# Kernel optimization log

Measured on AMD Instinct MI355X. Metric: run time of the kernel, lower is better.

## Reference

```python
import jax, jax.numpy as jnp
import numpy as np

VOCAB, EMBED, ZCH = 4096, 128, 256
B, H, W = 32, 16, 16


def setup_inputs() -> dict:
    key = jax.random.key(0)
    k1, k2, k3, k4 = jax.random.split(key, 4)
    z_e = jax.random.normal(k1, (B, ZCH, H, W), dtype=jnp.float32)
    pre_w = jax.random.normal(k2, (EMBED, ZCH), dtype=jnp.float32) * 0.02
    pre_b = jnp.zeros((EMBED,), dtype=jnp.float32)
    # codebook initialized uniform(-1/vocab, 1/vocab) like the torch module
    emb = jax.random.uniform(k3, (VOCAB, EMBED), dtype=jnp.float32,
                             minval=-1.0 / VOCAB, maxval=1.0 / VOCAB)
    post_w = jax.random.normal(k4, (ZCH, EMBED), dtype=jnp.float32) * 0.02
    post_b = jnp.zeros((ZCH,), dtype=jnp.float32)
    return {"z_e": z_e, "pre_w": pre_w, "pre_b": pre_b, "emb": emb,
            "post_w": post_w, "post_b": post_b}


def reference(z_e, pre_w, pre_b, emb, post_w, post_b):
    # pre_quant_conv: 1x1 conv == per-pixel linear, z_channels -> embed_dim
    z = jnp.einsum('bchw,ec->behw', z_e, pre_w) + pre_b[None, :, None, None]
    b, e, h, w = z.shape
    zf = z.transpose(0, 2, 3, 1).reshape(-1, e)                 # (b*h*w, e)
    # squared distance to all codebook vectors: |z|^2 + |c|^2 - 2 z.c
    dist = (jnp.sum(zf * zf, axis=1, keepdims=True)
            + jnp.sum(emb * emb, axis=1)
            - 2.0 * zf @ emb.T)                                  # (b*h*w, vocab)
    tokens = jnp.argmin(dist, axis=-1)                           # (b*h*w,)
    z_q = emb[tokens].reshape(b, h, w, e).transpose(0, 3, 1, 2)  # (b,e,h,w)
    # straight-through estimator
    dec_in = z + jax.lax.stop_gradient(z_q - z)
    # post_quant_conv: 1x1 conv embed_dim -> z_channels (decoder input)
    rec = jnp.einsum('behw,ce->bchw', dec_in, post_w) + post_b[None, :, None, None]
    return z, z_q, rec
```

## Files before the change

### kernel.cpp

```cpp
#include <hip/hip_runtime.h>
#include <hip/hip_bf16.h>
#include <cstdint>

#define NB   32
#define NC   256
#define NE   128
#define NS   256
#define NV   4096
#define NP   8192
#define NSPLIT 8

typedef unsigned short ushort_t;
typedef __attribute__((ext_vector_type(8))) short bf16x8;
typedef __attribute__((ext_vector_type(8))) unsigned short us8;
typedef __attribute__((ext_vector_type(4))) float f32x4;

__device__ __forceinline__ float bf2f(ushort_t u) {
    union { unsigned int i; float f; } x; x.i = ((unsigned int)u) << 16; return x.f;
}
__device__ __forceinline__ ushort_t f2bf(float f) {
    __hip_bfloat16 h = __float2bfloat16(f);
    ushort_t u; __builtin_memcpy(&u, &h, 2); return u;
}
__device__ __forceinline__ unsigned asu(float f) { unsigned u; __builtin_memcpy(&u,&f,4); return u; }
__device__ __forceinline__ float    asf(unsigned u) { float f; __builtin_memcpy(&f,&u,4); return f; }

__global__ __launch_bounds__(256) void pre_conv_pack(
    const float* __restrict__ z_e, const float* __restrict__ pre_w,
    const float* __restrict__ pre_b, const float* __restrict__ emb,
    float* __restrict__ out_z, ushort_t* __restrict__ Bpack,
    float* __restrict__ cnorm)
{
    __shared__ __align__(16) float wtile[16 * 256];
    __shared__ __align__(16) float part[4 * 16 * 64];

    const int t = threadIdx.x;

    if (blockIdx.x == 8) {
        const int v     = (blockIdx.y * 4 + blockIdx.z) * 32 + (t >> 3);
        const int chunk = t & 7;
        const float4* rp = (const float4*)(emb + (size_t)v * NE + chunk * 16);
        float4 x0 = rp[0], x1 = rp[1], x2 = rp[2], x3 = rp[3];
        float xs[16] = { x0.x, x0.y, x0.z, x0.w, x1.x, x1.y, x1.z, x1.w,
                         x2.x, x2.y, x2.z, x2.w, x3.x, x3.y, x3.z, x3.w };
        us8 h0, h1;
        float nn = 0.f;
#pragma unroll
        for (int j = 0; j < 8; j++) {
            nn = fmaf(xs[j], xs[j], nn);
            h0[j] = f2bf(xs[j]);
        }
#pragma unroll
        for (int j = 0; j < 8; j++) {
            nn = fmaf(xs[8 + j], xs[8 + j], nn);
            h1[j] = f2bf(xs[8 + j]);
        }
        nn += __shfl_xor(nn, 1);
        nn += __shfl_xor(nn, 2);
        nn += __shfl_xor(nn, 4);
        if (chunk == 0) cnorm[v] = 0.5f * nn;

        const int G  = v >> 4;
        const int ks = chunk >> 1;
        const int q0 = (chunk & 1) * 2;
        const int L0 = (v & 15) | (q0 << 4);
        const int L1 = (v & 15) | ((q0 + 1) << 4);
        *(us8*)(Bpack + ((size_t)G * 4 + ks) * 512 + L0 * 8) = h0;
        *(us8*)(Bpack + ((size_t)G * 4 + ks) * 512 + L1 * 8) = h1;
        return;
    }

    const int e0 = blockIdx.x * 16;
    const int b  = blockIdx.y;
    const int s0 = blockIdx.z * 64;

    for (int idx = t; idx < 16 * 256; idx += 256)
        wtile[idx] = pre_w[(e0 + (idx >> 8)) * 256 + (idx & 255)];
    __syncthreads();

    const int kq = t >> 6, sl = t & 63;
    float acc[16];
#pragma unroll
    for (int r = 0; r < 16; r++) acc[r] = 0.f;

    const float* zin = z_e + (size_t)(b * NC + kq * 64) * NS + s0 + sl;
    const int cb = kq * 64;
#pragma unroll 4
    for (int i = 0; i < 16; i++) {
        const int c = i * 4;
        float z0 = zin[(c + 0) * NS];
        float z1 = zin[(c + 1) * NS];
        float z2 = zin[(c + 2) * NS];
        float z3 = zin[(c + 3) * NS];
#pragma unroll
        for (int r = 0; r < 16; r++) {
            float4 w = *(const float4*)&wtile[r * 256 + cb + c];
            acc[r] = fmaf(z0, w.x, fmaf(z1, w.y, fmaf(z2, w.z, fmaf(z3, w.w, acc[r]))));
        }
    }
#pragma unroll
    for (int r = 0; r < 16; r++)
        part[(kq * 16 + r) * 64 + sl] = acc[r];
    __syncthreads();

    const int r4 = t >> 6, sl2 = t & 63;
#pragma unroll
    for (int j = 0; j < 4; j++) {
        const int r = j * 4 + r4;
        float v = pre_b[e0 + r]
                + part[(0 * 16 + r) * 64 + sl2]
                + part[(1 * 16 + r) * 64 + sl2]
                + part[(2 * 16 + r) * 64 + sl2]
                + part[(3 * 16 + r) * 64 + sl2];
        out_z[(size_t)(b * NE + e0 + r) * NS + s0 + sl2] = v;
    }
}

__global__ __launch_bounds__(256, 3) void score_mfma(
    const float* __restrict__ z, const ushort_t* __restrict__ Bpack,
    const float* __restrict__ cnorm, int* __restrict__ pidx4)
{
    __shared__ __align__(16) char smraw[40960];
    float* As  = (float*)smraw;
    float* r1  = (float*)smraw;
    float* r2  = (float*)(smraw + 16640);
    float* t4b = (float*)(smraw + 33280);

    const int t = threadIdx.x;
    const int wave = t >> 6, lane = t & 63;
    const int set = blockIdx.x;
    const int split = blockIdx.y;
    const int p0 = set * 64;
    const int b  = p0 >> 8;
    const int s0 = p0 & 255;

    for (int idx = t; idx < 64 * 128; idx += 256) {
        int k = idx >> 6, i = idx & 63;
        As[i * 132 + k] = z[(size_t)(b * NE + k) * NS + s0 + i];
    }
    __syncthreads();

    const int am = lane & 15, aq = lane >> 4;
    bf16x8 ah[4][4];
#pragma unroll
    for (int mt = 0; mt < 4; mt++)
#pragma unroll
        for (int ks = 0; ks < 4; ks++) {
            const unsigned* src = (const unsigned*)(As + (mt * 16 + am) * 132 + ks * 32 + aq * 8);
            union { unsigned u[4]; bf16x8 v; } pk;
#pragma unroll
            for (int pr = 0; pr < 4; pr++)
                pk.u[pr] = (src[2 * pr + 1] & 0xFFFF0000u) | (src[2 * pr] >> 16);
            ah[mt][ks] = pk.v;
        }
    __syncthreads();

    const int Gbase = split * 32 + wave * 8;
    float cn[8];
#pragma unroll
    for (int cgi = 0; cgi < 8; cgi++)
        cn[cgi] = cnorm[(Gbase + cgi) * 16 + am];

    float b1v[16], b2v[16];
#pragma unroll
    for (int i = 0; i < 16; i++) { b1v[i] = -1e30f; b2v[i] = -1e30f; }

    bf16x8 bh[4], bhn[4];
#pragma unroll
    for (int ks = 0; ks < 4; ks++)
        bh[ks] = *(const bf16x8*)(Bpack + ((size_t)Gbase * 4 + ks) * 512 + lane * 8);

    for (int cgi = 0; cgi < 8; cgi++) {
        if (cgi < 7) {
#pragma unroll
            for (int ks = 0; ks < 4; ks++)
                bhn[ks] = *(const bf16x8*)(Bpack + ((size_t)(Gbase + cgi + 1) * 4 + ks) * 512 + lane * 8);
        }

        f32x4 acc[4];
#pragma unroll
        for (int mt = 0; mt < 4; mt++) acc[mt] = (f32x4){0.f, 0.f, 0.f, 0.f};
#pragma unroll
        for (int ks = 0; ks < 4; ks++)
#pragma unroll
            for (int mt = 0; mt < 4; mt++)
                acc[mt] = __builtin_amdgcn_mfma_f32_16x16x32_bf16(ah[mt][ks], bh[ks], acc[mt], 0, 0, 0);

#pragma unroll
        for (int mt = 0; mt < 4; mt++)
#pragma unroll
            for (int reg = 0; reg < 4; reg++) {
                const int si = mt * 4 + reg;
                float sc = acc[mt][reg] - cn[cgi];
                float ev = asf((asu(sc) & ~7u) | (unsigned)cgi);
                b2v[si] = fmaxf(b2v[si], fminf(ev, b1v[si]));
                b1v[si] = fmaxf(b1v[si], ev);
            }
#pragma unroll
        for (int ks = 0; ks < 4; ks++) bh[ks] = bhn[ks];
    }

    const int slot = wave * 16 + am;
#pragma unroll
    for (int mt = 0; mt < 4; mt++)
#pragma unroll
        for (int reg = 0; reg < 4; reg++) {
            int px = mt * 16 + aq * 4 + reg;
            r1[slot * 65 + px] = b1v[mt * 4 + reg];
            r2[slot * 65 + px] = b2v[mt * 4 + reg];
        }
    __syncthreads();

    {
        const int px = t >> 2, ch = t & 3;
        float t1 = -1e30f, t2 = -1e30f, t3 = -1e30f, t4 = -1e30f;
        for (int i = 0; i < 16; i++) {
            int sl = ch * 16 + i;
#pragma unroll
            for (int e = 0; e < 2; e++) {
                float raw = e ? r2[sl * 65 + px] : r1[sl * 65 + px];
                unsigned vb = asu(raw);
                float v = asf((vb & ~511u) | ((unsigned)sl << 3) | (vb & 7u));
                t4 = fmaxf(t4, fminf(v, t3));
                t3 = fmaxf(t3, fminf(v, t2));
                t2 = fmaxf(t2, fminf(v, t1));
                t1 = fmaxf(t1, v);
            }
        }
        float* dst = t4b + (px * 4 + ch) * 4;
        dst[0] = t1; dst[1] = t2; dst[2] = t3; dst[3] = t4;
    }
    __syncthreads();

    if (t < 64) {
        float u1 = -1e30f, u2 = -1e30f, u3 = -1e30f, u4 = -1e30f;
        for (int ch = 0; ch < 4; ch++) {
#pragma unroll
            for (int j = 0; j < 4; j++) {
                float v = t4b[(t * 4 + ch) * 4 + j];
                u4 = fmaxf(u4, fminf(v, u3));
                u3 = fmaxf(u3, fminf(v, u2));
                u2 = fmaxf(u2, fminf(v, u1));
                u1 = fmaxf(u1, v);
            }
        }
        const int p = p0 + t;
        float uu[4] = { u1, u2, u3, u4 };
#pragma unroll
        for (int j = 0; j < 4; j++) {
            unsigned bits = asu(uu[j]) & 511u;
            int w = (int)(bits >> 7), res = (int)((bits >> 3) & 15u), cg = (int)(bits & 7u);
            pidx4[((size_t)split * NP + p) * 4 + j] = split * 512 + (w * 8 + cg) * 16 + res;
        }
    }
}

__global__ __launch_bounds__(256) void rescore_gather(
    const float* __restrict__ z, const float* __restrict__ emb,
    const int* __restrict__ pidx4, float* __restrict__ out_zq)
{
    __shared__ __align__(16) float zl[16 * 132];
    __shared__ double bsl[16 * 16];
    __shared__ int    bil[16 * 16];
    __shared__ int    tok[16];

    const int t  = threadIdx.x;
    const int p0 = blockIdx.x * 16;
    const int b  = p0 >> 8;
    const int s0 = p0 & 255;

    for (int idx = t; idx < 16 * 128; idx += 256) {
        int k = idx >> 4, i = idx & 15;
        zl[i * 132 + k] = z[(size_t)(b * NE + k) * NS + s0 + i];
    }
    __syncthreads();

    const int il = t >> 4;
    const int cc = t & 15;
    const int p  = p0 + il;
    double bs = -1e300; int bi = 0x7fffffff;
#pragma unroll
    for (int jj = 0; jj < 2; jj++) {
        int cand = cc * 2 + jj;
        int split = cand >> 2, slot = cand & 3;
        int idx = pidx4[((size_t)split * NP + p) * 4 + slot];
        const float* er = emb + (size_t)idx * NE;
        double dot = 0.0, nn = 0.0;
        for (int k = 0; k < NE; k += 4) {
            float4 e4 = *(const float4*)(er + k);
            dot += (double)zl[il * 132 + k + 0] * (double)e4.x;
            dot += (double)zl[il * 132 + k + 1] * (double)e4.y;
            dot += (double)zl[il * 132 + k + 2] * (double)e4.z;
            dot += (double)zl[il * 132 + k + 3] * (double)e4.w;
            nn  += (double)e4.x * e4.x + (double)e4.y * e4.y
                 + (double)e4.z * e4.z + (double)e4.w * e4.w;
        }
        double sc = dot - 0.5 * nn;
        if (sc > bs || (sc == bs && idx < bi)) { bs = sc; bi = idx; }
    }
    bsl[il * 16 + cc] = bs;
    bil[il * 16 + cc] = bi;
    __syncthreads();

    if (t < 16) {
        double B = -1e300; int I = 0x7fffffff;
        for (int c = 0; c < 16; c++) {
            double sc = bsl[t * 16 + c]; int ii = bil[t * 16 + c];
            if (sc > B || (sc == B && ii < I)) { B = sc; I = ii; }
        }
        tok[t] = I;
    }
    __syncthreads();

    for (int idx = t; idx < NE * 16; idx += 256) {
        int e = idx >> 4, i = idx & 15;
        out_zq[(size_t)(b * NE + e) * NS + s0 + i] = emb[(size_t)tok[i] * NE + e];
    }
}

__global__ __launch_bounds__(256) void post_conv(
    const float* __restrict__ zq, const float* __restrict__ post_w,
    const float* __restrict__ post_b, float* __restrict__ out_rec)
{
    __shared__ __align__(16) float wtile[16 * 128];
    __shared__ __align__(16) float part[4 * 16 * 64];

    const int t  = threadIdx.x;
    const int c0 = blockIdx.x * 16;
    const int b  = blockIdx.y;
    const int s0 = blockIdx.z * 64;

    for (int idx = t; idx < 16 * 128; idx += 256)
        wtile[idx] = post_w[(c0 + (idx >> 7)) * 128 + (idx & 127)];
    __syncthreads();

    const int kq = t >> 6, sl = t & 63;
    float acc[16];
#pragma unroll
    for (int r = 0; r < 16; r++) acc[r] = 0.f;

    const float* zin = zq + (size_t)(b * NE + kq * 32) * NS + s0 + sl;
    const int eb = kq * 32;
#pragma unroll 4
    for (int i = 0; i < 8; i++) {
        const int e = i * 4;
        float z0 = zin[(e + 0) * NS];
        float z1 = zin[(e + 1) * NS];
        float z2 = zin[(e + 2) * NS];
        float z3 = zin[(e + 3) * NS];
#pragma unroll
        for (int r = 0; r < 16; r++) {
            float4 w = *(const float4*)&wtile[r * 128 + eb + e];
            acc[r] = fmaf(z0, w.x, fmaf(z1, w.y, fmaf(z2, w.z, fmaf(z3, w.w, acc[r]))));
        }
    }
#pragma unroll
    for (int r = 0; r < 16; r++)
        part[(kq * 16 + r) * 64 + sl] = acc[r];
    __syncthreads();

    const int r4 = t >> 6, sl2 = t & 63;
#pragma unroll
    for (int j = 0; j < 4; j++) {
        const int r = j * 4 + r4;
        float v = post_b[c0 + r]
                + part[(0 * 16 + r) * 64 + sl2]
                + part[(1 * 16 + r) * 64 + sl2]
                + part[(2 * 16 + r) * 64 + sl2]
                + part[(3 * 16 + r) * 64 + sl2];
        out_rec[(size_t)(b * NC + c0 + r) * NS + s0 + sl2] = v;
    }
}

extern "C" void kernel_launch(void* const* d_in, const int* in_sizes, int n_in,
                              void* d_out, int out_size, void* d_ws, size_t ws_size,
                              hipStream_t stream)
{
    const float* z_e    = (const float*)d_in[0];
    const float* pre_w  = (const float*)d_in[1];
    const float* pre_b  = (const float*)d_in[2];
    const float* emb    = (const float*)d_in[3];
    const float* post_w = (const float*)d_in[4];
    const float* post_b = (const float*)d_in[5];

    float* out     = (float*)d_out;
    float* out_z   = out;
    float* out_zq  = out + 1048576;
    float* out_rec = out + 2097152;

    const size_t SZ_BPACK = (size_t)256 * 4 * 512 * 2;
    const size_t SZ_CNORM = (size_t)NV * 4;
    const size_t SZ_PIDX4 = (size_t)NSPLIT * NP * 4 * 4;
    const size_t NEED = SZ_BPACK + SZ_CNORM + SZ_PIDX4;
    char* scr = (ws_size >= NEED) ? (char*)d_ws : (char*)out_rec;
    ushort_t* Bpack = (ushort_t*)scr;
    float*    cnorm = (float*)(scr + SZ_BPACK);
    int*      pidx4 = (int*)(scr + SZ_BPACK + SZ_CNORM);

    pre_conv_pack <<<dim3(9, 32, 4),     256, 0, stream>>>(z_e, pre_w, pre_b, emb,
                                                           out_z, Bpack, cnorm);
    score_mfma    <<<dim3(128, NSPLIT),  256, 0, stream>>>(out_z, Bpack, cnorm, pidx4);
    rescore_gather<<<dim3(512),          256, 0, stream>>>(out_z, emb, pidx4, out_zq);
    post_conv     <<<dim3(16, 32, 4),    256, 0, stream>>>(out_zq, post_w, post_b, out_rec);
}
```

Before: 151.5 us.

## Fuse four VQ stages into one cooperative persistent kernel with grid syncs

Replaces the four separate launches (pre-conv/pack, MFMA scoring, rescore/gather, post-conv) with one cooperative kernel. The stages are separated by grid.sync and run as grid-stride loops over the same work units. The aim is to remove per-launch overhead and the inter-kernel gaps. The cost is grid-wide barriers, a persistent grid capped at 1024 blocks that may lower parallelism in some stages, and shared-memory sizing fixed to the largest stage. The old multi-kernel path stays as a fallback if the cooperative launch fails.

```diff
diff --git a/kernel.cpp b/kernel.cpp
--- a/kernel.cpp
+++ b/kernel.cpp
@@ -1,6 +1,9 @@
 #include <hip/hip_runtime.h>
 #include <hip/hip_bf16.h>
+#include <hip/hip_cooperative_groups.h>
 #include <cstdint>
+
+namespace cg = cooperative_groups;
 
 #define NB   32
 #define NC   256
@@ -25,6 +28,353 @@
 __device__ __forceinline__ unsigned asu(float f) { unsigned u; __builtin_memcpy(&u,&f,4); return u; }
 __device__ __forceinline__ float    asf(unsigned u) { float f; __builtin_memcpy(&f,&u,4); return f; }
 
+__global__ __launch_bounds__(256, 3) void vq_fused(
+    const float* __restrict__ z_e, const float* __restrict__ pre_w,
+    const float* __restrict__ pre_b, const float* __restrict__ emb,
+    const float* __restrict__ post_w, const float* __restrict__ post_b,
+    float* __restrict__ out_z, float* __restrict__ out_zq,
+    float* __restrict__ out_rec, ushort_t* __restrict__ Bpack,
+    float* __restrict__ cnorm, int* __restrict__ pidx4)
+{
+    cg::grid_group grid = cg::this_grid();
+    __shared__ __align__(16) char smraw[40960];
+    const int t = threadIdx.x;
+
+    for (int u = blockIdx.x; u < 1152; u += gridDim.x) {
+        if (u >= 1024) {
+            const int pu    = u - 1024;
+            const int v     = pu * 32 + (t >> 3);
+            const int chunk = t & 7;
+            const float4* rp = (const float4*)(emb + (size_t)v * NE + chunk * 16);
+            float4 x0 = rp[0], x1 = rp[1], x2 = rp[2], x3 = rp[3];
+            float xs[16] = { x0.x, x0.y, x0.z, x0.w, x1.x, x1.y, x1.z, x1.w,
+                             x2.x, x2.y, x2.z, x2.w, x3.x, x3.y, x3.z, x3.w };
+            us8 h0, h1;
+            float nn = 0.f;
+#pragma unroll
+            for (int j = 0; j < 8; j++) {
+                nn = fmaf(xs[j], xs[j], nn);
+                h0[j] = f2bf(xs[j]);
+            }
+#pragma unroll
+            for (int j = 0; j < 8; j++) {
+                nn = fmaf(xs[8 + j], xs[8 + j], nn);
+                h1[j] = f2bf(xs[8 + j]);
+            }
+            nn += __shfl_xor(nn, 1);
+            nn += __shfl_xor(nn, 2);
+            nn += __shfl_xor(nn, 4);
+            if (chunk == 0) cnorm[v] = 0.5f * nn;
+
+            const int G  = v >> 4;
+            const int ks = chunk >> 1;
+            const int q0 = (chunk & 1) * 2;
+            const int L0 = (v & 15) | (q0 << 4);
+            const int L1 = (v & 15) | ((q0 + 1) << 4);
+            *(us8*)(Bpack + ((size_t)G * 4 + ks) * 512 + L0 * 8) = h0;
+            *(us8*)(Bpack + ((size_t)G * 4 + ks) * 512 + L1 * 8) = h1;
+            continue;
+        }
+
+        float* wtile = (float*)smraw;
+        float* part  = (float*)(smraw + 16384);
+        const int e0 = (u >> 7) * 16;
+        const int b  = (u >> 2) & 31;
+        const int s0 = (u & 3) * 64;
+
+        __syncthreads();
+        for (int idx = t; idx < 16 * 256; idx += 256)
+            wtile[idx] = pre_w[(e0 + (idx >> 8)) * 256 + (idx & 255)];
+        __syncthreads();
+
+        const int kq = t >> 6, sl = t & 63;
+        float acc[16];
+#pragma unroll
+        for (int r = 0; r < 16; r++) acc[r] = 0.f;
+
+        const float* zin = z_e + (size_t)(b * NC + kq * 64) * NS + s0 + sl;
+        const int cb = kq * 64;
+#pragma unroll 4
+        for (int i = 0; i < 16; i++) {
+            const int c = i * 4;
+            float z0 = zin[(c + 0) * NS];
+            float z1 = zin[(c + 1) * NS];
+            float z2 = zin[(c + 2) * NS];
+            float z3 = zin[(c + 3) * NS];
+#pragma unroll
+            for (int r = 0; r < 16; r++) {
+                float4 w = *(const float4*)&wtile[r * 256 + cb + c];
+                acc[r] = fmaf(z0, w.x, fmaf(z1, w.y, fmaf(z2, w.z, fmaf(z3, w.w, acc[r]))));
+            }
+        }
+#pragma unroll
+        for (int r = 0; r < 16; r++)
+            part[(kq * 16 + r) * 64 + sl] = acc[r];
+        __syncthreads();
+
+        const int r4 = t >> 6, sl2 = t & 63;
+#pragma unroll
+        for (int j = 0; j < 4; j++) {
+            const int r = j * 4 + r4;
+            float v = pre_b[e0 + r]
+                    + part[(0 * 16 + r) * 64 + sl2]
+                    + part[(1 * 16 + r) * 64 + sl2]
+                    + part[(2 * 16 + r) * 64 + sl2]
+                    + part[(3 * 16 + r) * 64 + sl2];
+            out_z[(size_t)(b * NE + e0 + r) * NS + s0 + sl2] = v;
+        }
+    }
+    grid.sync();
+
+    for (int u = blockIdx.x; u < 1024; u += gridDim.x) {
+        float* As  = (float*)smraw;
+        float* r1  = (float*)smraw;
+        float* r2  = (float*)(smraw + 16640);
+        float* t4b = (float*)(smraw + 33280);
+
+        const int wave = t >> 6, lane = t & 63;
+        const int set   = u & 127;
+        const int split = u >> 7;
+        const int p0 = set * 64;
+        const int b  = p0 >> 8;
+        const int s0 = p0 & 255;
+
+        __syncthreads();
+        for (int idx = t; idx < 64 * 128; idx += 256) {
+            int k = idx >> 6, i = idx & 63;
+            As[i * 132 + k] = out_z[(size_t)(b * NE + k) * NS + s0 + i];
+        }
+        __syncthreads();
+
+        const int am = lane & 15, aq = lane >> 4;
+        bf16x8 ah[4][4];
+#pragma unroll
+        for (int mt = 0; mt < 4; mt++)
+#pragma unroll
+            for (int ks = 0; ks < 4; ks++) {
+                const unsigned* src = (const unsigned*)(As + (mt * 16 + am) * 132 + ks * 32 + aq * 8);
+                union { unsigned uu[4]; bf16x8 v; } pk;
+#pragma unroll
+                for (int pr = 0; pr < 4; pr++)
+                    pk.uu[pr] = (src[2 * pr + 1] & 0xFFFF0000u) | (src[2 * pr] >> 16);
+                ah[mt][ks] = pk.v;
+            }
+        __syncthreads();
+
+        const int Gbase = split * 32 + wave * 8;
+        float cn[8];
+#pragma unroll
+        for (int cgi = 0; cgi < 8; cgi++)
+            cn[cgi] = cnorm[(Gbase + cgi) * 16 + am];
+
+        float b1v[16], b2v[16];
+#pragma unroll
+        for (int i = 0; i < 16; i++) { b1v[i] = -1e30f; b2v[i] = -1e30f; }
+
+        bf16x8 bh[4], bhn[4];
+#pragma unroll
+        for (int ks = 0; ks < 4; ks++)
+            bh[ks] = *(const bf16x8*)(Bpack + ((size_t)Gbase * 4 + ks) * 512 + lane * 8);
+
+        for (int cgi = 0; cgi < 8; cgi++) {
+            if (cgi < 7) {
+#pragma unroll
+                for (int ks = 0; ks < 4; ks++)
+                    bhn[ks] = *(const bf16x8*)(Bpack + ((size_t)(Gbase + cgi + 1) * 4 + ks) * 512 + lane * 8);
+            }
+
+            f32x4 acc[4];
+#pragma unroll
+            for (int mt = 0; mt < 4; mt++) acc[mt] = (f32x4){0.f, 0.f, 0.f, 0.f};
+#pragma unroll
+            for (int ks = 0; ks < 4; ks++)
+#pragma unroll
+                for (int mt = 0; mt < 4; mt++)
+                    acc[mt] = __builtin_amdgcn_mfma_f32_16x16x32_bf16(ah[mt][ks], bh[ks], acc[mt], 0, 0, 0);
+
+#pragma unroll
+            for (int mt = 0; mt < 4; mt++)
+#pragma unroll
+                for (int reg = 0; reg < 4; reg++) {
+                    const int si = mt * 4 + reg;
+                    float sc = acc[mt][reg] - cn[cgi];
+                    float ev = asf((asu(sc) & ~7u) | (unsigned)cgi);
+                    b2v[si] = fmaxf(b2v[si], fminf(ev, b1v[si]));
+                    b1v[si] = fmaxf(b1v[si], ev);
+                }
+#pragma unroll
+            for (int ks = 0; ks < 4; ks++) bh[ks] = bhn[ks];
+        }
+
+        const int slot = wave * 16 + am;
+#pragma unroll
+        for (int mt = 0; mt < 4; mt++)
+#pragma unroll
+            for (int reg = 0; reg < 4; reg++) {
+                int px = mt * 16 + aq * 4 + reg;
+                r1[slot * 65 + px] = b1v[mt * 4 + reg];
+                r2[slot * 65 + px] = b2v[mt * 4 + reg];
+            }
+        __syncthreads();
+
+        {
+            const int px = t >> 2, ch = t & 3;
+            float t1 = -1e30f, t2 = -1e30f, t3 = -1e30f, t4 = -1e30f;
+            for (int i = 0; i < 16; i++) {
+                int sl = ch * 16 + i;
+#pragma unroll
+                for (int e = 0; e < 2; e++) {
+                    float raw = e ? r2[sl * 65 + px] : r1[sl * 65 + px];
+                    unsigned vb = asu(raw);
+                    float v = asf((vb & ~511u) | ((unsigned)sl << 3) | (vb & 7u));
+                    t4 = fmaxf(t4, fminf(v, t3));
+                    t3 = fmaxf(t3, fminf(v, t2));
+                    t2 = fmaxf(t2, fminf(v, t1));
+                    t1 = fmaxf(t1, v);
+                }
+            }
+            float* dst = t4b + (px * 4 + ch) * 4;
+            dst[0] = t1; dst[1] = t2; dst[2] = t3; dst[3] = t4;
+        }
+        __syncthreads();
+
+        if (t < 64) {
+            float u1 = -1e30f, u2 = -1e30f, u3 = -1e30f, u4 = -1e30f;
+            for (int ch = 0; ch < 4; ch++) {
+#pragma unroll
+                for (int j = 0; j < 4; j++) {
+                    float v = t4b[(t * 4 + ch) * 4 + j];
+                    u4 = fmaxf(u4, fminf(v, u3));
+                    u3 = fmaxf(u3, fminf(v, u2));
+                    u2 = fmaxf(u2, fminf(v, u1));
+                    u1 = fmaxf(u1, v);
+                }
+            }
+            const int p = p0 + t;
+            float uu[4] = { u1, u2, u3, u4 };
+#pragma unroll
+            for (int j = 0; j < 4; j++) {
+                unsigned bits = asu(uu[j]) & 511u;
+                int w = (int)(bits >> 7), res = (int)((bits >> 3) & 15u), cg2 = (int)(bits & 7u);
+                pidx4[((size_t)split * NP + p) * 4 + j] = split * 512 + (w * 8 + cg2) * 16 + res;
+            }
+        }
+    }
+    grid.sync();
+
+    for (int u = blockIdx.x; u < 512; u += gridDim.x) {
+        float*  zl  = (float*)smraw;
+        double* bsl = (double*)(smraw + 8448);
+        int*    bil = (int*)(smraw + 10496);
+        int*    tok = (int*)(smraw + 11520);
+
+        const int p0 = u * 16;
+        const int b  = p0 >> 8;
+        const int s0 = p0 & 255;
+
+        __syncthreads();
+        for (int idx = t; idx < 16 * 128; idx += 256) {
+            int k = idx >> 4, i = idx & 15;
+            zl[i * 132 + k] = out_z[(size_t)(b * NE + k) * NS + s0 + i];
+        }
+        __syncthreads();
+
+        const int il = t >> 4;
+        const int cc = t & 15;
+        const int p  = p0 + il;
+        double bs = -1e300; int bi = 0x7fffffff;
+#pragma unroll
+        for (int jj = 0; jj < 2; jj++) {
+            int cand = cc * 2 + jj;
+            int split = cand >> 2, slot = cand & 3;
+            int idx = pidx4[((size_t)split * NP + p) * 4 + slot];
+            const float* er = emb + (size_t)idx * NE;
+            double dot = 0.0, nn = 0.0;
+            for (int k = 0; k < NE; k += 4) {
+                float4 e4 = *(const float4*)(er + k);
+                dot += (double)zl[il * 132 + k + 0] * (double)e4.x;
+                dot += (double)zl[il * 132 + k + 1] * (double)e4.y;
+                dot += (double)zl[il * 132 + k + 2] * (double)e4.z;
+                dot += (double)zl[il * 132 + k + 3] * (double)e4.w;
+                nn  += (double)e4.x * e4.x + (double)e4.y * e4.y
+                     + (double)e4.z * e4.z + (double)e4.w * e4.w;
+            }
+            double sc = dot - 0.5 * nn;
+            if (sc > bs || (sc == bs && idx < bi)) { bs = sc; bi = idx; }
+        }
+        bsl[il * 16 + cc] = bs;
+        bil[il * 16 + cc] = bi;
+        __syncthreads();
+
+        if (t < 16) {
+            double B = -1e300; int I = 0x7fffffff;
+            for (int c = 0; c < 16; c++) {
+                double sc = bsl[t * 16 + c]; int ii = bil[t * 16 + c];
+                if (sc > B || (sc == B && ii < I)) { B = sc; I = ii; }
+            }
+            tok[t] = I;
+        }
+        __syncthreads();
+
+        for (int idx = t; idx < NE * 16; idx += 256) {
+            int e = idx >> 4, i = idx & 15;
+            out_zq[(size_t)(b * NE + e) * NS + s0 + i] = emb[(size_t)tok[i] * NE + e];
+        }
+    }
+    grid.sync();
+
+    for (int u = blockIdx.x; u < 2048; u += gridDim.x) {
+        float* wtile = (float*)smraw;
+        float* part  = (float*)(smraw + 8192);
+
+        const int c0 = (u >> 7) * 16;
+        const int b  = (u >> 2) & 31;
+        const int s0 = (u & 3) * 64;
+
+        __syncthreads();
+        for (int idx = t; idx < 16 * 128; idx += 256)
+            wtile[idx] = post_w[(c0 + (idx >> 7)) * 128 + (idx & 127)];
+        __syncthreads();
+
+        const int kq = t >> 6, sl = t & 63;
+        float acc[16];
+#pragma unroll
+        for (int r = 0; r < 16; r++) acc[r] = 0.f;
+
+        const float* zin = out_zq + (size_t)(b * NE + kq * 32) * NS + s0 + sl;
+        const int eb = kq * 32;
+#pragma unroll 4
+        for (int i = 0; i < 8; i++) {
+            const int e = i * 4;
+            float z0 = zin[(e + 0) * NS];
+            float z1 = zin[(e + 1) * NS];
+            float z2 = zin[(e + 2) * NS];
+            float z3 = zin[(e + 3) * NS];
+#pragma unroll
+            for (int r = 0; r < 16; r++) {
+                float4 w = *(const float4*)&wtile[r * 128 + eb + e];
+                acc[r] = fmaf(z0, w.x, fmaf(z1, w.y, fmaf(z2, w.z, fmaf(z3, w.w, acc[r]))));
+            }
+        }
+#pragma unroll
+        for (int r = 0; r < 16; r++)
+            part[(kq * 16 + r) * 64 + sl] = acc[r];
+        __syncthreads();
+
+        const int r4 = t >> 6, sl2 = t & 63;
+#pragma unroll
+        for (int j = 0; j < 4; j++) {
+            const int r = j * 4 + r4;
+            float v = post_b[c0 + r]
+                    + part[(0 * 16 + r) * 64 + sl2]
+                    + part[(1 * 16 + r) * 64 + sl2]
+                    + part[(2 * 16 + r) * 64 + sl2]
+                    + part[(3 * 16 + r) * 64 + sl2];
+            out_rec[(size_t)(b * NC + c0 + r) * NS + s0 + sl2] = v;
+        }
+    }
+}
+
 __global__ __launch_bounds__(256) void pre_conv_pack(
     const float* __restrict__ z_e, const float* __restrict__ pre_w,
     const float* __restrict__ pre_b, const float* __restrict__ emb,
@@ -46,15 +396,9 @@
         us8 h0, h1;
         float nn = 0.f;
 #pragma unroll
-        for (int j = 0; j < 8; j++) {
-            nn = fmaf(xs[j], xs[j], nn);
-            h0[j] = f2bf(xs[j]);
-        }
-#pragma unroll
-        for (int j = 0; j < 8; j++) {
-            nn = fmaf(xs[8 + j], xs[8 + j], nn);
-            h1[j] = f2bf(xs[8 + j]);
-        }
+        for (int j = 0; j < 8; j++) { nn = fmaf(xs[j], xs[j], nn); h0[j] = f2bf(xs[j]); }
+#pragma unroll
+        for (int j = 0; j < 8; j++) { nn = fmaf(xs[8 + j], xs[8 + j], nn); h1[j] = f2bf(xs[8 + j]); }
         nn += __shfl_xor(nn, 1);
         nn += __shfl_xor(nn, 2);
         nn += __shfl_xor(nn, 4);
@@ -397,9 +741,44 @@
     float*    cnorm = (float*)(scr + SZ_BPACK);
     int*      pidx4 = (int*)(scr + SZ_BPACK + SZ_CNORM);
 
-    pre_conv_pack <<<dim3(9, 32, 4),     256, 0, stream>>>(z_e, pre_w, pre_b, emb,
-                                                           out_z, Bpack, cnorm);
-    score_mfma    <<<dim3(128, NSPLIT),  256, 0, stream>>>(out_z, Bpack, cnorm, pidx4);
-    rescore_gather<<<dim3(512),          256, 0, stream>>>(out_z, emb, pidx4, out_zq);
-    post_conv     <<<dim3(16, 32, 4),    256, 0, stream>>>(out_zq, post_w, post_b, out_rec);
+    static int coopGrid = -1;
+    if (coopGrid < 0) {
+        int nb = 0;
+        if (hipOccupancyMaxActiveBlocksPerMultiprocessor(
+                &nb, (const void*)vq_fused, 256, 0) != hipSuccess || nb < 1)
+            nb = 0;
+        int cus = 256;
+        hipDeviceProp_t prop;
+        int dev = 0;
+        if (hipGetDevice(&dev) == hipSuccess &&
+            hipGetDeviceProperties(&prop, dev) == hipSuccess &&
+            prop.multiProcessorCount > 0)
+            cus = prop.multiProcessorCount;
+        coopGrid = nb * cus;
+        if (coopGrid > 1024) coopGrid = 1024;
+    }
+
+    bool launched = false;
+    if (coopGrid >= 1) {
+        void* args[] = { (void*)&z_e, (void*)&pre_w, (void*)&pre_b, (void*)&emb,
+                         (void*)&post_w, (void*)&post_b,
+                         (void*)&out_z, (void*)&out_zq, (void*)&out_rec,
+                         (void*)&Bpack, (void*)&cnorm, (void*)&pidx4 };
+        hipError_t err = hipLaunchCooperativeKernel(
+            (void*)vq_fused, dim3((unsigned)coopGrid), dim3(256), args, 0, stream);
+        if (err == hipSuccess) {
+            launched = true;
+        } else {
+            (void)hipGetLastError();
+            coopGrid = 0;
+        }
+    }
+
+    if (!launched) {
+        pre_conv_pack <<<dim3(9, 32, 4),     256, 0, stream>>>(z_e, pre_w, pre_b, emb,
+                                                               out_z, Bpack, cnorm);
+        score_mfma    <<<dim3(128, NSPLIT),  256, 0, stream>>>(out_z, Bpack, cnorm, pidx4);
+        rescore_gather<<<dim3(512),          256, 0, stream>>>(out_z, emb, pidx4, out_zq);
+        post_conv     <<<dim3(16, 32, 4),    256, 0, stream>>>(out_zq, post_w, post_b, out_rec);
+    }
 }
```

Result: slower. 341.8 us (+125.7%).

## Fuse post-quant conv into rescore/gather kernel to skip z_q reread

Applied to the files above, without the earlier changes.

Merges the post_conv kernel into rescore_gather. The gathered codebook rows are kept in shared memory and multiplied by post_w tiles loaded in four 64-channel chunks. This removes one kernel launch and the global re-read of z_q. In exchange each of the 512 blocks reloads the full post_w matrix (128 KB) and uses much more shared memory (about 45 KB), which may lower occupancy.

```diff
diff --git a/kernel.cpp b/kernel.cpp
--- a/kernel.cpp
+++ b/kernel.cpp
@@ -255,14 +255,19 @@
     }
 }
 
-__global__ __launch_bounds__(256) void rescore_gather(
+__global__ __launch_bounds__(256) void rescore_gather_post(
     const float* __restrict__ z, const float* __restrict__ emb,
-    const int* __restrict__ pidx4, float* __restrict__ out_zq)
+    const int* __restrict__ pidx4, const float* __restrict__ post_w,
+    const float* __restrict__ post_b, float* __restrict__ out_zq,
+    float* __restrict__ out_rec)
 {
     __shared__ __align__(16) float zl[16 * 132];
     __shared__ double bsl[16 * 16];
     __shared__ int    bil[16 * 16];
     __shared__ int    tok[16];
+    __shared__ __align__(16) float eg[16 * 132];
+    __shared__ __align__(16) float wtile[64 * 129];
+    __shared__ float  outb[64 * 17];
 
     const int t  = threadIdx.x;
     const int p0 = blockIdx.x * 16;
@@ -314,61 +319,54 @@
 
     for (int idx = t; idx < NE * 16; idx += 256) {
         int e = idx >> 4, i = idx & 15;
-        out_zq[(size_t)(b * NE + e) * NS + s0 + i] = emb[(size_t)tok[i] * NE + e];
-    }
-}
-
-__global__ __launch_bounds__(256) void post_conv(
-    const float* __restrict__ zq, const float* __restrict__ post_w,
-    const float* __restrict__ post_b, float* __restrict__ out_rec)
-{
-    __shared__ __align__(16) float wtile[16 * 128];
-    __shared__ __align__(16) float part[4 * 16 * 64];
-
-    const int t  = threadIdx.x;
-    const int c0 = blockIdx.x * 16;
-    const int b  = blockIdx.y;
-    const int s0 = blockIdx.z * 64;
-
-    for (int idx = t; idx < 16 * 128; idx += 256)
-        wtile[idx] = post_w[(c0 + (idx >> 7)) * 128 + (idx & 127)];
-    __syncthreads();
-
-    const int kq = t >> 6, sl = t & 63;
-    float acc[16];
-#pragma unroll
-    for (int r = 0; r < 16; r++) acc[r] = 0.f;
-
-    const float* zin = zq + (size_t)(b * NE + kq * 32) * NS + s0 + sl;
-    const int eb = kq * 32;
+        float v = emb[(size_t)tok[i] * NE + e];
+        out_zq[(size_t)(b * NE + e) * NS + s0 + i] = v;
+        eg[i * 132 + e] = v;
+    }
+    __syncthreads();
+
+    const int pg  = t >> 6;
+    const int cl  = t & 63;
+    const int px0 = pg * 4;
+    const float* g0 = &eg[(px0 + 0) * 132];
+    const float* g1 = &eg[(px0 + 1) * 132];
+    const float* g2 = &eg[(px0 + 2) * 132];
+    const float* g3 = &eg[(px0 + 3) * 132];
+
+    for (int ct = 0; ct < 4; ct++) {
+        for (int idx = t; idx < 64 * 128; idx += 256) {
+            int r = idx >> 7, k = idx & 127;
+            wtile[r * 129 + k] = post_w[(size_t)(ct * 64 + r) * 128 + k];
+        }
+        __syncthreads();
+
+        float a0 = 0.f, a1 = 0.f, a2 = 0.f, a3 = 0.f;
+        const float* wr = &wtile[cl * 129];
 #pragma unroll 4
-    for (int i = 0; i < 8; i++) {
-        const int e = i * 4;
-        float z0 = zin[(e + 0) * NS];
-        float z1 = zin[(e + 1) * NS];
-        float z2 = zin[(e + 2) * NS];
-        float z3 = zin[(e + 3) * NS];
-#pragma unroll
-        for (int r = 0; r < 16; r++) {
-            float4 w = *(const float4*)&wtile[r * 128 + eb + e];
-            acc[r] = fmaf(z0, w.x, fmaf(z1, w.y, fmaf(z2, w.z, fmaf(z3, w.w, acc[r]))));
-        }
-    }
-#pragma unroll
-    for (int r = 0; r < 16; r++)
-        part[(kq * 16 + r) * 64 + sl] = acc[r];
-    __syncthreads();
-
-    const int r4 = t >> 6, sl2 = t & 63;
-#pragma unroll
-    for (int j = 0; j < 4; j++) {
-        const int r = j * 4 + r4;
-        float v = post_b[c0 + r]
-                + part[(0 * 16 + r) * 64 + sl2]
-                + part[(1 * 16 + r) * 64 + sl2]
-                + part[(2 * 16 + r) * 64 + sl2]
-                + part[(3 * 16 + r) * 64 + sl2];
-        out_rec[(size_t)(b * NC + c0 + r) * NS + s0 + sl2] = v;
+        for (int k = 0; k < 128; k += 4) {
+            float w0 = wr[k + 0], w1 = wr[k + 1], w2 = wr[k + 2], w3 = wr[k + 3];
+            float4 q0 = *(const float4*)&g0[k];
+            float4 q1 = *(const float4*)&g1[k];
+            float4 q2 = *(const float4*)&g2[k];
+            float4 q3 = *(const float4*)&g3[k];
+            a0 = fmaf(w0, q0.x, fmaf(w1, q0.y, fmaf(w2, q0.z, fmaf(w3, q0.w, a0))));
+            a1 = fmaf(w0, q1.x, fmaf(w1, q1.y, fmaf(w2, q1.z, fmaf(w3, q1.w, a1))));
+            a2 = fmaf(w0, q2.x, fmaf(w1, q2.y, fmaf(w2, q2.z, fmaf(w3, q2.w, a2))));
+            a3 = fmaf(w0, q3.x, fmaf(w1, q3.y, fmaf(w2, q3.z, fmaf(w3, q3.w, a3))));
+        }
+        float bias = post_b[ct * 64 + cl];
+        outb[cl * 17 + px0 + 0] = a0 + bias;
+        outb[cl * 17 + px0 + 1] = a1 + bias;
+        outb[cl * 17 + px0 + 2] = a2 + bias;
+        outb[cl * 17 + px0 + 3] = a3 + bias;
+        __syncthreads();
+
+        for (int idx = t; idx < 64 * 16; idx += 256) {
+            int c_loc = idx >> 4, px = idx & 15;
+            out_rec[(size_t)(b * NC + ct * 64 + c_loc) * NS + s0 + px] =
+                outb[c_loc * 17 + px];
+        }
+        __syncthreads();
     }
 }
 
@@ -397,9 +395,10 @@
     float*    cnorm = (float*)(scr + SZ_BPACK);
     int*      pidx4 = (int*)(scr + SZ_BPACK + SZ_CNORM);
 
-    pre_conv_pack <<<dim3(9, 32, 4),     256, 0, stream>>>(z_e, pre_w, pre_b, emb,
-                                                           out_z, Bpack, cnorm);
-    score_mfma    <<<dim3(128, NSPLIT),  256, 0, stream>>>(out_z, Bpack, cnorm, pidx4);
-    rescore_gather<<<dim3(512),          256, 0, stream>>>(out_z, emb, pidx4, out_zq);
-    post_conv     <<<dim3(16, 32, 4),    256, 0, stream>>>(out_zq, post_w, post_b, out_rec);
-}
+    pre_conv_pack      <<<dim3(9, 32, 4),    256, 0, stream>>>(z_e, pre_w, pre_b, emb,
+                                                               out_z, Bpack, cnorm);
+    score_mfma         <<<dim3(128, NSPLIT), 256, 0, stream>>>(out_z, Bpack, cnorm, pidx4);
+    rescore_gather_post<<<dim3(512),         256, 0, stream>>>(out_z, emb, pidx4,
+                                                               post_w, post_b,
+                                                               out_zq, out_rec);
+}
```

Measured after the change: 158.6 us. 4.7% more time.
